# Kernel tuning notes

Measured on AMD Instinct MI355X. Metric: run time of the kernel, lower is better.

Reference implementation:

```python
import jax, jax.numpy as jnp
import numpy as np

EPS = 1e-5
BATCH_SIZE = 8
GROUP = 32
N_EDGE_TYPE = 7


def dual_gn(data, batch_id, w, b):
    # data: [N, C]; per-batch group-norm via scatter_add over batch_id
    N, C = data.shape
    cpg = C // GROUP  # channels per group

    def adjust(t):  # sum within each group, broadcast back to channels
        t = t.reshape(-1, GROUP, cpg).sum(-1, keepdims=True)
        return jnp.broadcast_to(t, (t.shape[0], GROUP, cpg)).reshape(-1, C)

    ones = jnp.ones((N,), data.dtype)
    count = jax.ops.segment_sum(ones, batch_id, num_segments=BATCH_SIZE) * cpg
    inv_count = 1.0 / (count + EPS)
    mean = adjust(jax.ops.segment_sum(data, batch_id, num_segments=BATCH_SIZE) * inv_count[:, None])
    out = data - mean[batch_id]
    var = adjust(jax.ops.segment_sum(out * out, batch_id, num_segments=BATCH_SIZE) * inv_count[:, None])
    inv_std = 1.0 / jnp.sqrt(var + EPS)
    return out * inv_std[batch_id] * w + b


def graph_conv(x, row, col, etype, W):
    # scatter_mean of neighbor features into per-(node, edge_type) buckets, then matmul
    N, C = x.shape
    idx = row * N_EDGE_TYPE + etype  # [E]
    gathered = x[col]  # [E, C]
    s = jax.ops.segment_sum(gathered, idx, num_segments=N * N_EDGE_TYPE)
    cnt = jax.ops.segment_sum(jnp.ones((col.shape[0],), x.dtype), idx, num_segments=N * N_EDGE_TYPE)
    col_data = s / jnp.maximum(cnt, 1.0)[:, None]  # [N*7, C], scatter_mean (empty buckets -> 0)
    return col_data.reshape(N, N_EDGE_TYPE * C) @ W  # [N, C_out]


def silu(x):
    return x * jax.nn.sigmoid(x)


def setup_inputs() -> dict:
    key = jax.random.key(0)
    ks = jax.random.split(key, 10)
    N, C, E = 100000, 256, 700000
    x = jax.random.normal(ks[0], (N, C), dtype=jnp.float32)
    edge_index = jax.random.randint(ks[1], (2, E), 0, N)
    edge_type = jax.random.randint(ks[2], (E,), 0, N_EDGE_TYPE)
    batch_id = jnp.sort(jax.random.randint(ks[3], (N,), 0, BATCH_SIZE))
    a = np.sqrt(3.0) * np.sqrt(2.0 / float(7 * C + 7 * C))
    conv1_w = jax.random.uniform(ks[4], (N_EDGE_TYPE * C, C), dtype=jnp.float32, minval=-a, maxval=a)
    conv2_w = jax.random.uniform(ks[5], (N_EDGE_TYPE * C, C), dtype=jnp.float32, minval=-a, maxval=a)
    gn1_w = jnp.ones((1, C), jnp.float32)
    gn1_b = jnp.zeros((1, C), jnp.float32)
    gn2_w = jnp.ones((1, C), jnp.float32)
    gn2_b = jnp.zeros((1, C), jnp.float32)
    return {"x": x, "gn1_w": gn1_w, "gn1_b": gn1_b, "conv1_w": conv1_w,
            "gn2_w": gn2_w, "gn2_b": gn2_b, "conv2_w": conv2_w,
            "edge_index": edge_index, "edge_type": edge_type, "batch_id": batch_id}


def reference(x, gn1_w, gn1_b, conv1_w, gn2_w, gn2_b, conv2_w, edge_index, edge_type, batch_id):
    row, col = edge_index[0], edge_index[1]
    h = dual_gn(x, batch_id, gn1_w, gn1_b)
    h = silu(h)
    h = graph_conv(h, row, col, edge_type, conv1_w)
    h = dual_gn(h, batch_id, gn2_w, gn2_b)
    h = silu(h)  # dropout p=0 -> identity
    h = graph_conv(h, row, col, edge_type, conv2_w)
    return h + x  # channel_in == channel_out: identity shortcut
```

## Files before the change

### kernel.cpp

```cpp
#include <hip/hip_runtime.h>
#include <hip/hip_bf16.h>
#include <cstdint>
#include <cstddef>

#define CCH 256
#define NTY 7
#define NBATCH 8
#define NGRP 32
#define CPG 8
#define KDIM (CCH*NTY)
#define GBM 128
#define GBN 256
#define GBK 32
#define EPT 4
#define SCAN_ITEMS 8
#define SROWS 128

typedef short short8 __attribute__((ext_vector_type(8)));
typedef float f32x4 __attribute__((ext_vector_type(4)));

__device__ __forceinline__ float bf2f(unsigned short u){
  return __uint_as_float(((unsigned)u) << 16);
}
__device__ __forceinline__ unsigned short f2bf(float f){
  unsigned u = __float_as_uint(f);
  u += 0x7fffu + ((u >> 16) & 1u);
  return (unsigned short)(u >> 16);
}

__device__ __forceinline__ bool probe_bf(const unsigned short* probe){
  return probe[0] == 0x3F80u;
}

__device__ __forceinline__ float ldd(const void* p, size_t i, bool isbf){
  return isbf ? bf2f(((const unsigned short*)p)[i]) : ((const float*)p)[i];
}
__device__ __forceinline__ void ld4d(const void* p, size_t i, bool isbf, float v[4]){
  if (isbf){
    ushort4 u = *(const ushort4*)((const unsigned short*)p + i);
    v[0]=bf2f(u.x); v[1]=bf2f(u.y); v[2]=bf2f(u.z); v[3]=bf2f(u.w);
  } else {
    float4 f = *(const float4*)((const float*)p + i);
    v[0]=f.x; v[1]=f.y; v[2]=f.z; v[3]=f.w;
  }
}

__device__ __forceinline__ void gload16(const unsigned short* g, short* lds_base){
  __builtin_amdgcn_global_load_lds(
      (const __attribute__((address_space(1))) unsigned int*)g,
      (__attribute__((address_space(3))) unsigned int*)lds_base,
      16, 0, 0);
}

__global__ void transpose_w(const void* __restrict__ W,
                            unsigned short* __restrict__ Wt,
                            const unsigned short* __restrict__ probe){
  bool isbf = probe_bf(probe);
  int k = blockIdx.x;
  int n = threadIdx.x;
  unsigned short v;
  if (isbf) v = ((const unsigned short*)W)[(size_t)k*CCH + n];
  else      v = f2bf(((const float*)W)[(size_t)k*CCH + n]);
  Wt[(size_t)n*KDIM + k] = v;
}

__global__ void batch_bounds(const int* __restrict__ bid, float* __restrict__ bcnt, int N){
  int b = threadIdx.x;
  if (b < NBATCH){
    int lo = 0, hi = N;
    while (lo < hi){ int mid = (lo+hi)>>1; if (bid[mid] < b) lo = mid+1; else hi = mid; }
    int b1 = b + 1;
    int lo2 = 0, hi2 = N;
    while (lo2 < hi2){ int mid = (lo2+hi2)>>1; if (bid[mid] < b1) lo2 = mid+1; else hi2 = mid; }
    bcnt[b] = (float)(lo2 - lo);
  }
}

__global__ void count_kernel(const int* __restrict__ row, const int* __restrict__ et,
                             int* __restrict__ bc, int N, int E){
  int base = blockIdx.x*blockDim.x*EPT + threadIdx.x;
  #pragma unroll
  for (int j = 0; j < EPT; ++j){
    int e = base + j*blockDim.x;
    if (e < E) atomicAdd(&bc[et[e]*N + row[e]], 1);
  }
}

__global__ void scan_block(const int* __restrict__ bc, int* __restrict__ seg_off,
                           int* __restrict__ bsum, int M){
  __shared__ int sd[256];
  int tid = threadIdx.x;
  int base = blockIdx.x*256*SCAN_ITEMS + tid*SCAN_ITEMS;
  int v[SCAN_ITEMS];
  int s = 0;
  #pragma unroll
  for (int j = 0; j < SCAN_ITEMS; ++j){
    int i = base + j;
    v[j] = (i < M) ? bc[i] : 0;
    s += v[j];
  }
  sd[tid] = s;
  __syncthreads();
  #pragma unroll
  for (int d = 1; d < 256; d <<= 1){
    int t = (tid >= d) ? sd[tid - d] : 0;
    __syncthreads();
    sd[tid] += t;
    __syncthreads();
  }
  int excl = sd[tid] - s;
  #pragma unroll
  for (int j = 0; j < SCAN_ITEMS; ++j){
    int i = base + j;
    if (i < M) seg_off[i] = excl;
    excl += v[j];
  }
  if (tid == 255) bsum[blockIdx.x] = sd[255];
}

__global__ void scan_mid(int* __restrict__ bsum, int* __restrict__ seg_off,
                         int nblk, int M){
  __shared__ int sd[1024];
  int tid = threadIdx.x;
  int val = (tid < nblk) ? bsum[tid] : 0;
  sd[tid] = val;
  __syncthreads();
  #pragma unroll
  for (int d = 1; d < 1024; d <<= 1){
    int t = (tid >= d) ? sd[tid - d] : 0;
    __syncthreads();
    sd[tid] += t;
    __syncthreads();
  }
  int excl = sd[tid] - val;
  if (tid < nblk) bsum[tid] = excl;
  if (tid == nblk - 1) seg_off[M] = excl + val;
}

__global__ void scan_add(int* __restrict__ seg_off, int* __restrict__ cursor,
                         const int* __restrict__ bsum, int M){
  int i = blockIdx.x*blockDim.x + threadIdx.x;
  if (i < M){
    int v = seg_off[i] + bsum[i >> 11];
    seg_off[i] = v;
    cursor[i] = v;
  }
}

__global__ void sort_kernel(const int* __restrict__ row, const int* __restrict__ col,
                            const int* __restrict__ et, int* __restrict__ cursor,
                            int* __restrict__ col_s, int N, int E){
  int base = blockIdx.x*blockDim.x*EPT + threadIdx.x;
  #pragma unroll
  for (int j = 0; j < EPT; ++j){
    int e = base + j*blockDim.x;
    if (e < E){
      int pos = atomicAdd(&cursor[et[e]*N + row[e]], 1);
      col_s[pos] = col[e];
    }
  }
}

__global__ void invcnt_kernel(const int* __restrict__ bc, float* __restrict__ icnt, int M){
  int i = blockIdx.x*blockDim.x + threadIdx.x;
  if (i < M) icnt[i] = 1.0f / fmaxf((float)bc[i], 1.0f);
}

__global__ void stats_kernel(const void* __restrict__ x, const int* __restrict__ bid,
                             float* __restrict__ S1, float* __restrict__ S2,
                             int N, const unsigned short* __restrict__ probe){
  __shared__ float sd1[256][4];
  __shared__ float sd2[256][4];
  bool isbf = probe ? probe_bf(probe) : false;
  int r0 = blockIdx.x * SROWS;
  if (r0 >= N) return;
  int r1 = min(N, r0 + SROWS);
  int tid = threadIdx.x;
  int c4 = (tid & 63) << 2;
  int ro = tid >> 6;
  int b0 = bid[r0], b1 = bid[r1 - 1];
  float a1[4] = {0.f,0.f,0.f,0.f}, a2[4] = {0.f,0.f,0.f,0.f};

  if (b0 == b1 && (r1 - r0) == SROWS){
    for (int rr = r0 + ro; rr < r1; rr += 32){
      float v[8][4];
      #pragma unroll
      for (int s = 0; s < 8; ++s)
        ld4d(x, (size_t)(rr + s*4)*CCH + c4, isbf, v[s]);
      #pragma unroll
      for (int s = 0; s < 8; ++s)
        #pragma unroll
        for (int j = 0; j < 4; ++j){ a1[j] += v[s][j]; a2[j] += v[s][j]*v[s][j]; }
    }
    #pragma unroll
    for (int j = 0; j < 4; ++j){ sd1[tid][j] = a1[j]; sd2[tid][j] = a2[j]; }
    __syncthreads();
    if (tid < 64){
      #pragma unroll
      for (int j = 0; j < 4; ++j){
        float t1 = sd1[tid][j] + sd1[tid+64][j] + sd1[tid+128][j] + sd1[tid+192][j];
        float t2 = sd2[tid][j] + sd2[tid+64][j] + sd2[tid+128][j] + sd2[tid+192][j];
        unsafeAtomicAdd(&S1[b0*CCH + (tid<<2) + j], t1);
        unsafeAtomicAdd(&S2[b0*CCH + (tid<<2) + j], t2);
      }
    }
  } else {
    int cur = b0;
    for (int rr = r0 + ro; rr < r1; rr += 4){
      int b = bid[rr];
      if (b != cur){
        #pragma unroll
        for (int j = 0; j < 4; ++j){
          unsafeAtomicAdd(&S1[cur*CCH + c4 + j], a1[j]);
          unsafeAtomicAdd(&S2[cur*CCH + c4 + j], a2[j]);
          a1[j] = 0.f; a2[j] = 0.f;
        }
        cur = b;
      }
      float v[4]; ld4d(x, (size_t)rr*CCH + c4, isbf, v);
      #pragma unroll
      for (int j = 0; j < 4; ++j){ a1[j] += v[j]; a2[j] += v[j]*v[j]; }
    }
    #pragma unroll
    for (int j = 0; j < 4; ++j){
      unsafeAtomicAdd(&S1[cur*CCH + c4 + j], a1[j]);
      unsafeAtomicAdd(&S2[cur*CCH + c4 + j], a2[j]);
    }
  }
}

__global__ void finalize_stats(const float* __restrict__ S1, const float* __restrict__ S2,
                               const float* __restrict__ bcnt,
                               float* __restrict__ meanv, float* __restrict__ istdv){
  int t = threadIdx.x;
  int b = t >> 5, g = t & 31;
  float g1 = 0.f, g2 = 0.f;
  #pragma unroll
  for (int j = 0; j < CPG; ++j){
    g1 += S1[b*CCH + g*CPG + j];
    g2 += S2[b*CCH + g*CPG + j];
  }
  float cntf = bcnt[b] * (float)CPG;
  float ic = 1.0f / (cntf + 1e-5f);
  float mean = g1 * ic;
  float var = (g2 - 2.f*mean*g1 + cntf*mean*mean) * ic;
  var = fmaxf(var, 0.f);
  meanv[t] = mean;
  istdv[t] = 1.0f / sqrtf(var + 1e-5f);
}

__global__ void norm_silu(const void* __restrict__ x, const int* __restrict__ bid,
                          const void* __restrict__ w, const void* __restrict__ bb,
                          const float* __restrict__ meanv, const float* __restrict__ istdv,
                          unsigned short* __restrict__ out, int N,
                          const unsigned short* __restrict__ probe, int x_internal){
  bool wbf = probe_bf(probe);
  bool xbf = x_internal ? false : wbf;
  int total = N * (CCH/4);
  for (int i = blockIdx.x*blockDim.x + threadIdx.x; i < total; i += gridDim.x*blockDim.x){
    int r  = i >> 6;
    int c4 = (i & 63) << 2;
    int b  = bid[r];
    int g  = c4 >> 3;
    float mean = meanv[b*NGRP + g];
    float istd = istdv[b*NGRP + g];
    float xv[4], wv[4], bv[4];
    ld4d(x, (size_t)r*CCH + c4, xbf, xv);
    ld4d(w, c4, wbf, wv);
    ld4d(bb, c4, wbf, bv);
    ushort4 o;
    unsigned short* op = &o.x;
    #pragma unroll
    for (int j = 0; j < 4; ++j){
      float v = (xv[j] - mean) * istd * wv[j] + bv[j];
      v = v / (1.0f + __expf(-v));
      op[j] = f2bf(v);
    }
    *(ushort4*)(out + (size_t)r*CCH + c4) = o;
  }
}

__global__ void build_a(const unsigned short* __restrict__ h,
                        const int* __restrict__ col_s,
                        const int* __restrict__ seg_off,
                        const float* __restrict__ icnt,
                        unsigned short* __restrict__ At,
                        int N, int row0, int nrows, int nrows_pad){
  int w = (blockIdx.x*blockDim.x + threadIdx.x) >> 6;
  int l = threadIdx.x & 63;
  if (w >= nrows_pad * NTY) return;
  int rr = w / NTY;
  int t  = w - rr * NTY;
  unsigned short* out = At + (size_t)rr*KDIM + t*CCH + l*4;
  if (rr >= nrows){
    *(ushort4*)out = (ushort4){0,0,0,0};
    return;
  }
  int idx = t*N + (row0 + rr);
  int s = seg_off[idx], e = seg_off[idx+1];
  float ax = 0.f, ay = 0.f, az = 0.f, aw = 0.f;
  for (int p = s; p < e; ++p){
    int c = col_s[p];
    ushort4 u = *(const ushort4*)(h + (size_t)c*CCH + l*4);
    ax += bf2f(u.x); ay += bf2f(u.y); az += bf2f(u.z); aw += bf2f(u.w);
  }
  float sc = icnt[idx];
  ushort4 o;
  o.x = f2bf(ax*sc); o.y = f2bf(ay*sc); o.z = f2bf(az*sc); o.w = f2bf(aw*sc);
  *(ushort4*)out = o;
}

__global__ __launch_bounds__(512)
void gemm_dense(const unsigned short* __restrict__ At,
                const unsigned short* __restrict__ Wt,
                const int* __restrict__ bid,
                float* __restrict__ S1, float* __restrict__ S2,
                float* __restrict__ accv,
                const void* __restrict__ xres,
                void* __restrict__ outp,
                const unsigned short* __restrict__ probe,
                int N, int row0, int nrows, int mode){
  __shared__ __align__(16) short As[GBM*GBK];
  __shared__ __align__(16) short Bs[GBN*GBK];

  int mb = blockIdx.x * GBM;
  int tid = threadIdx.x;
  int wv = tid >> 6, l = tid & 63;
  int lm = l & 15, lq = l >> 4;
  int wm = wv >> 2, wn = wv & 3;

  f32x4 acc[4][4];
  #pragma unroll
  for (int a = 0; a < 4; ++a)
    #pragma unroll
    for (int b = 0; b < 4; ++b)
      acc[a][b] = (f32x4){0.f,0.f,0.f,0.f};

  int srow  = wv*16 + (l >> 2);
  int skoff = (l & 3) * 8;
  const unsigned short* gA  = At + (size_t)(mb + srow)*KDIM + skoff;
  const unsigned short* gB0 = Wt + (size_t)srow*KDIM + skoff;
  const unsigned short* gB1 = Wt + (size_t)(128 + srow)*KDIM + skoff;
  short* lA  = &As[wv*512];
  short* lB0 = &Bs[wv*512];
  short* lB1 = &Bs[4096 + wv*512];

  for (int kt = 0; kt < KDIM/GBK; ++kt){
    int k0 = kt * GBK;
    __syncthreads();
    gload16(gA  + k0, lA);
    gload16(gB0 + k0, lB0);
    gload16(gB1 + k0, lB1);
    __syncthreads();
    short8 af[4], bfr[4];
    #pragma unroll
    for (int mt = 0; mt < 4; ++mt)
      af[mt] = *(const short8*)(&As[(wm*64 + mt*16 + lm)*GBK + lq*8]);
    #pragma unroll
    for (int nt = 0; nt < 4; ++nt)
      bfr[nt] = *(const short8*)(&Bs[(wn*64 + nt*16 + lm)*GBK + lq*8]);
    #pragma unroll
    for (int mt = 0; mt < 4; ++mt)
      #pragma unroll
      for (int nt = 0; nt < 4; ++nt)
        acc[mt][nt] = __builtin_amdgcn_mfma_f32_16x16x32_bf16(af[mt], bfr[nt], acc[mt][nt], 0, 0, 0);
  }

  int gmb = row0 + mb;
  if (mode == 1){
    int bA = bid[gmb];
    int rlast = min(gmb + GBM - 1, row0 + nrows - 1);
    int bB = bid[rlast];
    if (bB <= bA + 1){
      float s1a[4] = {0,0,0,0}, s2a[4] = {0,0,0,0};
      float s1b[4] = {0,0,0,0}, s2b[4] = {0,0,0,0};
      #pragma unroll
      for (int mt = 0; mt < 4; ++mt){
        int lb2 = mb + wm*64 + mt*16 + lq*4;
        #pragma unroll
        for (int r = 0; r < 4; ++r){
          int lr = lb2 + r;
          if (lr < nrows){
            int rg = row0 + lr;
            bool isA = (bid[rg] == bA);
            #pragma unroll
            for (int nt = 0; nt < 4; ++nt){
              float v = acc[mt][nt][r];
              accv[(size_t)rg*CCH + wn*64 + nt*16 + lm] = v;
              if (isA){ s1a[nt] += v; s2a[nt] += v*v; }
              else    { s1b[nt] += v; s2b[nt] += v*v; }
            }
          }
        }
      }
      #pragma unroll
      for (int nt = 0; nt < 4; ++nt){
        s1a[nt] += __shfl_xor(s1a[nt], 16); s1a[nt] += __shfl_xor(s1a[nt], 32);
        s2a[nt] += __shfl_xor(s2a[nt], 16); s2a[nt] += __shfl_xor(s2a[nt], 32);
        s1b[nt] += __shfl_xor(s1b[nt], 16); s1b[nt] += __shfl_xor(s1b[nt], 32);
        s2b[nt] += __shfl_xor(s2b[nt], 16); s2b[nt] += __shfl_xor(s2b[nt], 32);
      }
      if (lq == 0){
        #pragma unroll
        for (int nt = 0; nt < 4; ++nt){
          int cg = wn*64 + nt*16 + lm;
          unsafeAtomicAdd(&S1[bA*CCH + cg], s1a[nt]);
          unsafeAtomicAdd(&S2[bA*CCH + cg], s2a[nt]);
          if (bB != bA){
            unsafeAtomicAdd(&S1[bB*CCH + cg], s1b[nt]);
            unsafeAtomicAdd(&S2[bB*CCH + cg], s2b[nt]);
          }
        }
      }
    } else {
      #pragma unroll
      for (int mt = 0; mt < 4; ++mt){
        int lb2 = mb + wm*64 + mt*16 + lq*4;
        #pragma unroll
        for (int r = 0; r < 4; ++r){
          int lr = lb2 + r;
          if (lr < nrows){
            int rg = row0 + lr;
            int b = bid[rg];
            #pragma unroll
            for (int nt = 0; nt < 4; ++nt){
              float v = acc[mt][nt][r];
              int cg = wn*64 + nt*16 + lm;
              accv[(size_t)rg*CCH + cg] = v;
              unsafeAtomicAdd(&S1[b*CCH + cg], v);
              unsafeAtomicAdd(&S2[b*CCH + cg], v*v);
            }
          }
        }
      }
    }
  } else {
    bool isbf = probe_bf(probe);
    #pragma unroll
    for (int mt = 0; mt < 4; ++mt){
      int lb2 = mb + wm*64 + mt*16 + lq*4;
      #pragma unroll
      for (int r = 0; r < 4; ++r){
        int lr = lb2 + r;
        if (lr < nrows){
          int rg = row0 + lr;
          #pragma unroll
          for (int nt = 0; nt < 4; ++nt){
            int cg = wn*64 + nt*16 + lm;
            float v = acc[mt][nt][r] + ldd(xres, (size_t)rg*CCH + cg, isbf);
            if (isbf) ((unsigned short*)outp)[(size_t)rg*CCH + cg] = f2bf(v);
            else      ((float*)outp)[(size_t)rg*CCH + cg] = v;
          }
        }
      }
    }
  }
}

extern "C" void kernel_launch(void* const* d_in, const int* in_sizes, int n_in,
                              void* d_out, int out_size, void* d_ws, size_t ws_size,
                              hipStream_t stream){
  const void* x   = d_in[0];
  const unsigned short* g1w = (const unsigned short*)d_in[1];
  const void* g1b = d_in[2];
  const void* w1  = d_in[3];
  const void* g2w = d_in[4];
  const void* g2b = d_in[5];
  const void* w2  = d_in[6];
  const int* eidx  = (const int*)d_in[7];
  const int* etype = (const int*)d_in[8];
  const int* bid   = (const int*)d_in[9];

  const int N = in_sizes[0] / CCH;
  const int E = in_sizes[8];
  const int M = NTY * N;
  const int* row  = eidx;
  const int* colv = eidx + E;
  const unsigned short* probe = g1w;

  char* ws = (char*)d_ws;
  size_t off = 0;
  auto alloc = [&](size_t bytes) -> void* {
    void* p = ws + off;
    off += (bytes + 255) & ~(size_t)255;
    return p;
  };
  float* acc   = (float*)alloc((size_t)N*CCH*4);
  unsigned short* hbuf = (unsigned short*)alloc((size_t)N*CCH*2);
  int*   bc     = (int*)alloc((size_t)M*4);
  float* icnt   = (float*)alloc((size_t)M*4);
  int*   seg_off= (int*)alloc((size_t)(M+1)*4);
  int*   cursor = (int*)alloc((size_t)M*4);
  int*   col_s  = (int*)alloc((size_t)E*4);
  int*   bsum   = (int*)alloc(4096*4);
  unsigned short* Wt1 = (unsigned short*)alloc((size_t)KDIM*CCH*2);
  unsigned short* Wt2 = (unsigned short*)alloc((size_t)KDIM*CCH*2);
  float* S1 = (float*)alloc(NBATCH*CCH*4);
  float* S2 = (float*)alloc(NBATCH*CCH*4);
  float* bcn = (float*)alloc(NBATCH*4);
  float* meanv = (float*)alloc(NBATCH*NGRP*4);
  float* istdv = (float*)alloc(NBATCH*NGRP*4);

  const int Npad = (N + GBM - 1) & ~(GBM - 1);
  size_t avail = (ws_size > off) ? (ws_size - off) : 0;
  long atr_l = (long)(avail / ((size_t)KDIM * 2));
  int at_rows;
  if (atr_l >= (long)Npad) at_rows = Npad;
  else                     at_rows = (int)(atr_l & ~(long)(GBM - 1));
  if (at_rows < GBM) at_rows = GBM;
  unsigned short* At = (unsigned short*)(ws + off);

  const int cs_grid = (E + 256*EPT - 1) / (256*EPT);
  const int scan_nblk = (M + 2047) / 2048;
  const int stats_grid = (N + SROWS - 1) / SROWS;
  const size_t statbytes = (size_t)NBATCH*CCH*4*2;

  transpose_w<<<KDIM, CCH, 0, stream>>>(w1, Wt1, probe);
  transpose_w<<<KDIM, CCH, 0, stream>>>(w2, Wt2, probe);
  batch_bounds<<<1, 64, 0, stream>>>(bid, bcn, N);

  hipMemsetAsync(bc, 0, (size_t)M*4, stream);
  count_kernel<<<cs_grid, 256, 0, stream>>>(row, etype, bc, N, E);
  scan_block<<<scan_nblk, 256, 0, stream>>>(bc, seg_off, bsum, M);
  scan_mid<<<1, 1024, 0, stream>>>(bsum, seg_off, scan_nblk, M);
  scan_add<<<(M + 255)/256, 256, 0, stream>>>(seg_off, cursor, bsum, M);
  sort_kernel<<<cs_grid, 256, 0, stream>>>(row, colv, etype, cursor, col_s, N, E);
  invcnt_kernel<<<(M + 255)/256, 256, 0, stream>>>(bc, icnt, M);

  hipMemsetAsync(S1, 0, statbytes, stream);
  stats_kernel<<<stats_grid, 256, 0, stream>>>(x, bid, S1, S2, N, probe);
  finalize_stats<<<1, 256, 0, stream>>>(S1, S2, bcn, meanv, istdv);
  norm_silu<<<4096, 256, 0, stream>>>(x, bid, g1w, g1b, meanv, istdv, hbuf, N, probe, 0);

  hipMemsetAsync(S1, 0, statbytes, stream);
  for (int c0 = 0; c0 < N; c0 += at_rows){
    int nr = min(at_rows, N - c0);
    int nrp = (nr + GBM - 1) & ~(GBM - 1);
    int bwaves = nrp * NTY;
    build_a<<<(bwaves + 3)/4, 256, 0, stream>>>(hbuf, col_s, seg_off, icnt, At, N, c0, nr, nrp);
    gemm_dense<<<nrp/GBM, 512, 0, stream>>>(At, Wt1, bid, S1, S2, acc,
                                            nullptr, nullptr, probe, N, c0, nr, 1);
  }

  finalize_stats<<<1, 256, 0, stream>>>(S1, S2, bcn, meanv, istdv);
  norm_silu<<<4096, 256, 0, stream>>>(acc, bid, g2w, g2b, meanv, istdv, hbuf, N, probe, 1);

  for (int c0 = 0; c0 < N; c0 += at_rows){
    int nr = min(at_rows, N - c0);
    int nrp = (nr + GBM - 1) & ~(GBM - 1);
    int bwaves = nrp * NTY;
    build_a<<<(bwaves + 3)/4, 256, 0, stream>>>(hbuf, col_s, seg_off, icnt, At, N, c0, nr, nrp);
    gemm_dense<<<nrp/GBM, 512, 0, stream>>>(At, Wt2, bid, nullptr, nullptr, nullptr,
                                            x, d_out, probe, N, c0, nr, 2);
  }
}
```

Baseline: 1.351 ms.

## Reorder graph conv as per-type transform then gather instead of gather then GEMM

Uses linearity to compute P = h @ W_t for each edge type first, then gathers and averages the transformed rows per destination node. The old path built a large aggregated A matrix of width 7*C and ran a K=1792 GEMM. The new GEMM has K=256 but a 7x wider output, and the gather now reads bf16 P rows instead of h rows. The fused group-norm statistics in the GEMM epilogue are replaced by a separate stats pass over acc. Type chunks are sized to the available workspace, with accumulation into acc and the residual add in the last chunk. This reorders the rounding, since the transform outputs are stored in bf16 before averaging.

After: 1.172 ms. 1.15x faster.

```diff
diff --git a/kernel.cpp b/kernel.cpp
--- a/kernel.cpp
+++ b/kernel.cpp
@@ -52,16 +52,18 @@
       16, 0, 0);
 }
 
-__global__ void transpose_w(const void* __restrict__ W,
-                            unsigned short* __restrict__ Wt,
-                            const unsigned short* __restrict__ probe){
+__global__ void transpose_bt(const void* __restrict__ W,
+                             unsigned short* __restrict__ BT,
+                             const unsigned short* __restrict__ probe){
   bool isbf = probe_bf(probe);
-  int k = blockIdx.x;
-  int n = threadIdx.x;
+  int np = blockIdx.x;
+  int k  = threadIdx.x;
+  int t = np >> 8, n = np & 255;
+  size_t src = (size_t)(t*CCH + k)*CCH + n;
   unsigned short v;
-  if (isbf) v = ((const unsigned short*)W)[(size_t)k*CCH + n];
-  else      v = f2bf(((const float*)W)[(size_t)k*CCH + n]);
-  Wt[(size_t)n*KDIM + k] = v;
+  if (isbf) v = ((const unsigned short*)W)[src];
+  else      v = f2bf(((const float*)W)[src]);
+  BT[(size_t)np*CCH + k] = v;
 }
 
 __global__ void batch_bounds(const int* __restrict__ bid, float* __restrict__ bcnt, int N){
@@ -280,50 +282,15 @@
   }
 }
 
-__global__ void build_a(const unsigned short* __restrict__ h,
-                        const int* __restrict__ col_s,
-                        const int* __restrict__ seg_off,
-                        const float* __restrict__ icnt,
-                        unsigned short* __restrict__ At,
-                        int N, int row0, int nrows, int nrows_pad){
-  int w = (blockIdx.x*blockDim.x + threadIdx.x) >> 6;
-  int l = threadIdx.x & 63;
-  if (w >= nrows_pad * NTY) return;
-  int rr = w / NTY;
-  int t  = w - rr * NTY;
-  unsigned short* out = At + (size_t)rr*KDIM + t*CCH + l*4;
-  if (rr >= nrows){
-    *(ushort4*)out = (ushort4){0,0,0,0};
-    return;
-  }
-  int idx = t*N + (row0 + rr);
-  int s = seg_off[idx], e = seg_off[idx+1];
-  float ax = 0.f, ay = 0.f, az = 0.f, aw = 0.f;
-  for (int p = s; p < e; ++p){
-    int c = col_s[p];
-    ushort4 u = *(const ushort4*)(h + (size_t)c*CCH + l*4);
-    ax += bf2f(u.x); ay += bf2f(u.y); az += bf2f(u.z); aw += bf2f(u.w);
-  }
-  float sc = icnt[idx];
-  ushort4 o;
-  o.x = f2bf(ax*sc); o.y = f2bf(ay*sc); o.z = f2bf(az*sc); o.w = f2bf(aw*sc);
-  *(ushort4*)out = o;
-}
-
 __global__ __launch_bounds__(512)
-void gemm_dense(const unsigned short* __restrict__ At,
-                const unsigned short* __restrict__ Wt,
-                const int* __restrict__ bid,
-                float* __restrict__ S1, float* __restrict__ S2,
-                float* __restrict__ accv,
-                const void* __restrict__ xres,
-                void* __restrict__ outp,
-                const unsigned short* __restrict__ probe,
-                int N, int row0, int nrows, int mode){
+void gemm_p(const unsigned short* __restrict__ h,
+            const unsigned short* __restrict__ BTg,
+            unsigned short* __restrict__ P, int pstride){
   __shared__ __align__(16) short As[GBM*GBK];
   __shared__ __align__(16) short Bs[GBN*GBK];
 
   int mb = blockIdx.x * GBM;
+  int colbase = blockIdx.y * GBN;
   int tid = threadIdx.x;
   int wv = tid >> 6, l = tid & 63;
   int lm = l & 15, lq = l >> 4;
@@ -338,14 +305,14 @@
 
   int srow  = wv*16 + (l >> 2);
   int skoff = (l & 3) * 8;
-  const unsigned short* gA  = At + (size_t)(mb + srow)*KDIM + skoff;
-  const unsigned short* gB0 = Wt + (size_t)srow*KDIM + skoff;
-  const unsigned short* gB1 = Wt + (size_t)(128 + srow)*KDIM + skoff;
+  const unsigned short* gA  = h   + (size_t)(mb + srow)*CCH + skoff;
+  const unsigned short* gB0 = BTg + (size_t)(colbase + srow)*CCH + skoff;
+  const unsigned short* gB1 = BTg + (size_t)(colbase + 128 + srow)*CCH + skoff;
   short* lA  = &As[wv*512];
   short* lB0 = &Bs[wv*512];
   short* lB1 = &Bs[4096 + wv*512];
 
-  for (int kt = 0; kt < KDIM/GBK; ++kt){
+  for (int kt = 0; kt < CCH/GBK; ++kt){
     int k0 = kt * GBK;
     __syncthreads();
     gload16(gA  + k0, lA);
@@ -366,94 +333,78 @@
         acc[mt][nt] = __builtin_amdgcn_mfma_f32_16x16x32_bf16(af[mt], bfr[nt], acc[mt][nt], 0, 0, 0);
   }
 
-  int gmb = row0 + mb;
-  if (mode == 1){
-    int bA = bid[gmb];
-    int rlast = min(gmb + GBM - 1, row0 + nrows - 1);
-    int bB = bid[rlast];
-    if (bB <= bA + 1){
-      float s1a[4] = {0,0,0,0}, s2a[4] = {0,0,0,0};
-      float s1b[4] = {0,0,0,0}, s2b[4] = {0,0,0,0};
-      #pragma unroll
-      for (int mt = 0; mt < 4; ++mt){
-        int lb2 = mb + wm*64 + mt*16 + lq*4;
-        #pragma unroll
-        for (int r = 0; r < 4; ++r){
-          int lr = lb2 + r;
-          if (lr < nrows){
-            int rg = row0 + lr;
-            bool isA = (bid[rg] == bA);
-            #pragma unroll
-            for (int nt = 0; nt < 4; ++nt){
-              float v = acc[mt][nt][r];
-              accv[(size_t)rg*CCH + wn*64 + nt*16 + lm] = v;
-              if (isA){ s1a[nt] += v; s2a[nt] += v*v; }
-              else    { s1b[nt] += v; s2b[nt] += v*v; }
-            }
-          }
-        }
-      }
+  #pragma unroll
+  for (int mt = 0; mt < 4; ++mt){
+    int rbase = mb + wm*64 + mt*16 + lq*4;
+    #pragma unroll
+    for (int r = 0; r < 4; ++r){
       #pragma unroll
       for (int nt = 0; nt < 4; ++nt){
-        s1a[nt] += __shfl_xor(s1a[nt], 16); s1a[nt] += __shfl_xor(s1a[nt], 32);
-        s2a[nt] += __shfl_xor(s2a[nt], 16); s2a[nt] += __shfl_xor(s2a[nt], 32);
-        s1b[nt] += __shfl_xor(s1b[nt], 16); s1b[nt] += __shfl_xor(s1b[nt], 32);
-        s2b[nt] += __shfl_xor(s2b[nt], 16); s2b[nt] += __shfl_xor(s2b[nt], 32);
+        int cg = colbase + wn*64 + nt*16 + lm;
+        P[(size_t)(rbase + r)*pstride + cg] = f2bf(acc[mt][nt][r]);
       }
-      if (lq == 0){
-        #pragma unroll
-        for (int nt = 0; nt < 4; ++nt){
-          int cg = wn*64 + nt*16 + lm;
-          unsafeAtomicAdd(&S1[bA*CCH + cg], s1a[nt]);
-          unsafeAtomicAdd(&S2[bA*CCH + cg], s2a[nt]);
-          if (bB != bA){
-            unsafeAtomicAdd(&S1[bB*CCH + cg], s1b[nt]);
-            unsafeAtomicAdd(&S2[bB*CCH + cg], s2b[nt]);
-          }
-        }
-      }
+    }
+  }
+}
+
+__global__ void gather_out(const unsigned short* __restrict__ P,
+                           const int* __restrict__ col_s,
+                           const int* __restrict__ seg_off,
+                           const float* __restrict__ icnt,
+                           float* __restrict__ accv,
+                           const void* __restrict__ xres,
+                           void* __restrict__ outp,
+                           const unsigned short* __restrict__ probe,
+                           int N, int ntypes, int pstride, int mode){
+  int r = (blockIdx.x*blockDim.x + threadIdx.x) >> 6;
+  if (r >= N) return;
+  int l = threadIdx.x & 63;
+
+  int s[NTY], e[NTY]; float sc[NTY];
+  #pragma unroll
+  for (int t = 0; t < NTY; ++t){
+    if (t < ntypes){
+      int idx = t*N + r;
+      s[t]  = seg_off[idx];
+      e[t]  = seg_off[idx + 1];
+      sc[t] = icnt[idx];
+    } else { s[t] = 0; e[t] = 0; sc[t] = 0.f; }
+  }
+
+  float a0 = 0.f, a1 = 0.f, a2 = 0.f, a3 = 0.f;
+  #pragma unroll
+  for (int t = 0; t < NTY; ++t){
+    if (t >= ntypes) break;
+    float t0 = 0.f, t1 = 0.f, t2 = 0.f, t3 = 0.f;
+    for (int p = s[t]; p < e[t]; ++p){
+      int c = col_s[p];
+      ushort4 u = *(const ushort4*)(P + (size_t)c*pstride + t*CCH + l*4);
+      t0 += bf2f(u.x); t1 += bf2f(u.y); t2 += bf2f(u.z); t3 += bf2f(u.w);
+    }
+    a0 += sc[t]*t0; a1 += sc[t]*t1; a2 += sc[t]*t2; a3 += sc[t]*t3;
+  }
+
+  float* ap = accv + (size_t)r*CCH + l*4;
+  if (mode & 1){
+    float4 pa = *(const float4*)ap;
+    a0 += pa.x; a1 += pa.y; a2 += pa.z; a3 += pa.w;
+  }
+  if (mode & 2){
+    bool isbf = probe_bf(probe);
+    float xv[4];
+    ld4d(xres, (size_t)r*CCH + l*4, isbf, xv);
+    float r0 = a0 + xv[0], r1 = a1 + xv[1], r2 = a2 + xv[2], r3 = a3 + xv[3];
+    if (isbf){
+      ushort4 o;
+      o.x = f2bf(r0); o.y = f2bf(r1); o.z = f2bf(r2); o.w = f2bf(r3);
+      *(ushort4*)((unsigned short*)outp + (size_t)r*CCH + l*4) = o;
     } else {
-      #pragma unroll
-      for (int mt = 0; mt < 4; ++mt){
-        int lb2 = mb + wm*64 + mt*16 + lq*4;
-        #pragma unroll
-        for (int r = 0; r < 4; ++r){
-          int lr = lb2 + r;
-          if (lr < nrows){
-            int rg = row0 + lr;
-            int b = bid[rg];
-            #pragma unroll
-            for (int nt = 0; nt < 4; ++nt){
-              float v = acc[mt][nt][r];
-              int cg = wn*64 + nt*16 + lm;
-              accv[(size_t)rg*CCH + cg] = v;
-              unsafeAtomicAdd(&S1[b*CCH + cg], v);
-              unsafeAtomicAdd(&S2[b*CCH + cg], v*v);
-            }
-          }
-        }
-      }
+      float4 o = {r0, r1, r2, r3};
+      *(float4*)((float*)outp + (size_t)r*CCH + l*4) = o;
     }
   } else {
-    bool isbf = probe_bf(probe);
-    #pragma unroll
-    for (int mt = 0; mt < 4; ++mt){
-      int lb2 = mb + wm*64 + mt*16 + lq*4;
-      #pragma unroll
-      for (int r = 0; r < 4; ++r){
-        int lr = lb2 + r;
-        if (lr < nrows){
-          int rg = row0 + lr;
-          #pragma unroll
-          for (int nt = 0; nt < 4; ++nt){
-            int cg = wn*64 + nt*16 + lm;
-            float v = acc[mt][nt][r] + ldd(xres, (size_t)rg*CCH + cg, isbf);
-            if (isbf) ((unsigned short*)outp)[(size_t)rg*CCH + cg] = f2bf(v);
-            else      ((float*)outp)[(size_t)rg*CCH + cg] = v;
-          }
-        }
-      }
-    }
+    float4 o = {a0, a1, a2, a3};
+    *(float4*)ap = o;
   }
 }
 
@@ -474,6 +425,7 @@
   const int N = in_sizes[0] / CCH;
   const int E = in_sizes[8];
   const int M = NTY * N;
+  const int Npad = (N + GBM - 1) & ~(GBM - 1);
   const int* row  = eidx;
   const int* colv = eidx + E;
   const unsigned short* probe = g1w;
@@ -486,37 +438,36 @@
     return p;
   };
   float* acc   = (float*)alloc((size_t)N*CCH*4);
-  unsigned short* hbuf = (unsigned short*)alloc((size_t)N*CCH*2);
+  unsigned short* hbuf = (unsigned short*)alloc((size_t)Npad*CCH*2);
   int*   bc     = (int*)alloc((size_t)M*4);
   float* icnt   = (float*)alloc((size_t)M*4);
   int*   seg_off= (int*)alloc((size_t)(M+1)*4);
   int*   cursor = (int*)alloc((size_t)M*4);
   int*   col_s  = (int*)alloc((size_t)E*4);
   int*   bsum   = (int*)alloc(4096*4);
-  unsigned short* Wt1 = (unsigned short*)alloc((size_t)KDIM*CCH*2);
-  unsigned short* Wt2 = (unsigned short*)alloc((size_t)KDIM*CCH*2);
+  unsigned short* BT1 = (unsigned short*)alloc((size_t)KDIM*CCH*2);
+  unsigned short* BT2 = (unsigned short*)alloc((size_t)KDIM*CCH*2);
   float* S1 = (float*)alloc(NBATCH*CCH*4);
   float* S2 = (float*)alloc(NBATCH*CCH*4);
   float* bcn = (float*)alloc(NBATCH*4);
   float* meanv = (float*)alloc(NBATCH*NGRP*4);
   float* istdv = (float*)alloc(NBATCH*NGRP*4);
 
-  const int Npad = (N + GBM - 1) & ~(GBM - 1);
   size_t avail = (ws_size > off) ? (ws_size - off) : 0;
-  long atr_l = (long)(avail / ((size_t)KDIM * 2));
-  int at_rows;
-  if (atr_l >= (long)Npad) at_rows = Npad;
-  else                     at_rows = (int)(atr_l & ~(long)(GBM - 1));
-  if (at_rows < GBM) at_rows = GBM;
-  unsigned short* At = (unsigned short*)(ws + off);
+  const size_t type_bytes = (size_t)Npad * CCH * 2;
+  int types_fit = (int)(avail / type_bytes);
+  if (types_fit < 1) types_fit = 1;
+  if (types_fit > NTY) types_fit = NTY;
+  unsigned short* P = (unsigned short*)(ws + off);
 
   const int cs_grid = (E + 256*EPT - 1) / (256*EPT);
   const int scan_nblk = (M + 2047) / 2048;
   const int stats_grid = (N + SROWS - 1) / SROWS;
+  const int go_grid = (N*64 + 255) / 256;
   const size_t statbytes = (size_t)NBATCH*CCH*4*2;
 
-  transpose_w<<<KDIM, CCH, 0, stream>>>(w1, Wt1, probe);
-  transpose_w<<<KDIM, CCH, 0, stream>>>(w2, Wt2, probe);
+  transpose_bt<<<KDIM, CCH, 0, stream>>>(w1, BT1, probe);
+  transpose_bt<<<KDIM, CCH, 0, stream>>>(w2, BT2, probe);
   batch_bounds<<<1, 64, 0, stream>>>(bid, bcn, N);
 
   hipMemsetAsync(bc, 0, (size_t)M*4, stream);
@@ -532,25 +483,31 @@
   finalize_stats<<<1, 256, 0, stream>>>(S1, S2, bcn, meanv, istdv);
   norm_silu<<<4096, 256, 0, stream>>>(x, bid, g1w, g1b, meanv, istdv, hbuf, N, probe, 0);
 
+  for (int t0 = 0; t0 < NTY; t0 += types_fit){
+    int nt = min(types_fit, NTY - t0);
+    int pstride = nt * CCH;
+    dim3 g(Npad/GBM, nt);
+    gemm_p<<<g, 512, 0, stream>>>(hbuf, BT1 + (size_t)t0*CCH*CCH, P, pstride);
+    int mode = (t0 > 0) ? 1 : 0;
+    gather_out<<<go_grid, 256, 0, stream>>>(P, col_s, seg_off + (size_t)t0*N,
+                                            icnt + (size_t)t0*N, acc,
+                                            nullptr, nullptr, probe, N, nt, pstride, mode);
+  }
+
   hipMemsetAsync(S1, 0, statbytes, stream);
-  for (int c0 = 0; c0 < N; c0 += at_rows){
-    int nr = min(at_rows, N - c0);
-    int nrp = (nr + GBM - 1) & ~(GBM - 1);
-    int bwaves = nrp * NTY;
-    build_a<<<(bwaves + 3)/4, 256, 0, stream>>>(hbuf, col_s, seg_off, icnt, At, N, c0, nr, nrp);
-    gemm_dense<<<nrp/GBM, 512, 0, stream>>>(At, Wt1, bid, S1, S2, acc,
-                                            nullptr, nullptr, probe, N, c0, nr, 1);
-  }
-
+  stats_kernel<<<stats_grid, 256, 0, stream>>>(acc, bid, S1, S2, N, nullptr);
   finalize_stats<<<1, 256, 0, stream>>>(S1, S2, bcn, meanv, istdv);
   norm_silu<<<4096, 256, 0, stream>>>(acc, bid, g2w, g2b, meanv, istdv, hbuf, N, probe, 1);
 
-  for (int c0 = 0; c0 < N; c0 += at_rows){
-    int nr = min(at_rows, N - c0);
-    int nrp = (nr + GBM - 1) & ~(GBM - 1);
-    int bwaves = nrp * NTY;
-    build_a<<<(bwaves + 3)/4, 256, 0, stream>>>(hbuf, col_s, seg_off, icnt, At, N, c0, nr, nrp);
-    gemm_dense<<<nrp/GBM, 512, 0, stream>>>(At, Wt2, bid, nullptr, nullptr, nullptr,
-                                            x, d_out, probe, N, c0, nr, 2);
-  }
-}
+  for (int t0 = 0; t0 < NTY; t0 += types_fit){
+    int nt = min(types_fit, NTY - t0);
+    int pstride = nt * CCH;
+    bool last = (t0 + nt >= NTY);
+    dim3 g(Npad/GBM, nt);
+    gemm_p<<<g, 512, 0, stream>>>(hbuf, BT2 + (size_t)t0*CCH*CCH, P, pstride);
+    int mode = (last ? 2 : 0) | ((t0 > 0) ? 1 : 0);
+    gather_out<<<go_grid, 256, 0, stream>>>(P, col_s, seg_off + (size_t)t0*N,
+                                            icnt + (size_t)t0*N, acc,
+                                            x, d_out, probe, N, nt, pstride, mode);
+  }
+}
```
